# Performance work log

Measured on AMD Instinct MI355X. Metric: run time of the kernel, lower is better.

## Reference

```python
import jax, jax.numpy as jnp
import numpy as np

B = 131072      # batch
IN = 1024       # input_dim
H = 384         # hidden[0]
L = 128         # latent_dim = hidden[1]
K = 32          # slots_k
R = 2           # top_r
TAU = 0.7


def setup_inputs() -> dict:
    key = jax.random.key(0)
    ks = jax.random.split(key, 8)
    s = 0.02
    f32 = jnp.float32
    return {
        "x":  jax.random.normal(ks[0], (B, IN), f32),
        "w1": jax.random.normal(ks[1], (IN, H), f32) * s,
        "b1": jnp.zeros((H,), f32),
        "w2": jax.random.normal(ks[2], (H, L), f32) * s,
        "b2": jnp.zeros((L,), f32),
        "mk": jax.random.normal(ks[3], (K, L), f32) * s,  # memory_keys
        "mv": jax.random.normal(ks[4], (K, L), f32) * s,  # memory_values
        "w3": jax.random.normal(ks[5], (2 * L, H), f32) * s,
        "b3": jnp.zeros((H,), f32),
        "w4": jax.random.normal(ks[6], (H, 1), f32) * s,
        "b4": jnp.zeros((1,), f32),
    }


def reference(x, w1, b1, w2, b2, mk, mv, w3, b3, w4, b4):
    # block_a: Linear -> GELU -> (Dropout=id in eval) -> Linear -> GELU
    z = jax.nn.gelu(x @ w1 + b1, approximate=False)
    z = jax.nn.gelu(z @ w2 + b2, approximate=False)          # [B, L]

    # top-r slot attention over memory bank
    logits = (z @ mk.T) / TAU                                 # [B, K]
    _, idx = jax.lax.top_k(logits, R)                         # [B, R]
    keep = jax.nn.one_hot(idx, K, dtype=logits.dtype).sum(-2) > 0  # [B, K] bool
    masked = jnp.where(keep, logits, -jnp.inf)
    attn = jax.nn.softmax(masked, axis=-1)                    # [B, K]
    mem = attn @ mv                                           # [B, L]

    fused = jnp.concatenate([z, mem], axis=-1)                # [B, 2L]

    # default head: Linear -> GELU -> Linear(.,1)
    h = jax.nn.gelu(fused @ w3 + b3, approximate=False)
    logit = (h @ w4 + b4)[..., 0]                             # [B]
    return jax.nn.sigmoid(logit)
```

## Files before the change

kernel.cpp:

```cpp
#include <hip/hip_runtime.h>

#define BATCH   131072
#define INDIM   1024
#define BM      64
#define BDIM    512
#define NBLK    (BATCH / BM)

#define WT0_OFF  0
#define WT1_OFF  24576
#define XTA_OFF  49152
#define XTB_OFF  57344
#define Z1_OFF   0
#define W2T0_OFF 50176
#define W2T1_OFF 58368
#define FZ_OFF   0
#define RP_OFF   33792
#define W3T_OFF  42240
#define CB_OFF   66816
#define B1S_OFF  (CB_OFF)
#define B2S_OFF  (CB_OFF + 1536)
#define B3S_OFF  (CB_OFF + 2048)
#define W4S_OFF  (CB_OFF + 3584)
#define MKS_OFF  (CB_OFF + 5120)
#define SMEM_BYTES (CB_OFF + 13824)

typedef unsigned short u16;
typedef u16    u16x8  __attribute__((ext_vector_type(8)));
typedef u16    u16x4  __attribute__((ext_vector_type(4)));
typedef __bf16 bf16x8 __attribute__((ext_vector_type(8)));
typedef __bf16 bf16x4 __attribute__((ext_vector_type(4)));
typedef float  f32x4  __attribute__((ext_vector_type(4)));

__device__ __forceinline__ u16 f2bf(float f) {
  unsigned u = __float_as_uint(f);
  u += 0x7FFFu + ((u >> 16) & 1u);
  return (u16)(u >> 16);
}

__device__ __forceinline__ float gelu_fast(float v) {
  float t = v * v;
  float u = v * fmaf(t, 0.0356774081f, 0.7978845608f);
  float e = __builtin_amdgcn_exp2f(u * -2.885390082f);
  return v * __builtin_amdgcn_rcpf(1.0f + e);
}

__device__ __forceinline__ f32x4 mfma16(u16x8 a, u16x8 b, f32x4 c) {
  return __builtin_amdgcn_mfma_f32_16x16x32_bf16(
      __builtin_bit_cast(bf16x8, a), __builtin_bit_cast(bf16x8, b), c, 0, 0, 0);
}

__device__ __forceinline__ u16x8 cvt8(float4 a, float4 b) {
  bf16x8 r;
  r[0]=(__bf16)a.x; r[1]=(__bf16)a.y; r[2]=(__bf16)a.z; r[3]=(__bf16)a.w;
  r[4]=(__bf16)b.x; r[5]=(__bf16)b.y; r[6]=(__bf16)b.z; r[7]=(__bf16)b.w;
  return __builtin_bit_cast(u16x8, r);
}
__device__ __forceinline__ u16x4 cvt4(float4 a) {
  bf16x4 r;
  r[0]=(__bf16)a.x; r[1]=(__bf16)a.y; r[2]=(__bf16)a.z; r[3]=(__bf16)a.w;
  return __builtin_bit_cast(u16x4, r);
}

typedef __attribute__((address_space(3))) unsigned int       lds_u32;
typedef __attribute__((address_space(1))) const unsigned int glb_u32;
__device__ __forceinline__ void gload16(const void* g, void* l) {
  __builtin_amdgcn_global_load_lds((glb_u32*)g, (lds_u32*)l, 16, 0, 0);
}

#define FENCE_SCHED __builtin_amdgcn_sched_barrier(0)
#define WAIT_LGKM0 do { asm volatile("s_waitcnt lgkmcnt(0)" ::: "memory"); FENCE_SCHED; } while (0)
#define WAIT_VMN(N) do { asm volatile("s_waitcnt vmcnt(" #N ")" ::: "memory"); FENCE_SCHED; } while (0)
#define BARRIER_LGKM do { \
  asm volatile("s_waitcnt lgkmcnt(0)" ::: "memory"); \
  __builtin_amdgcn_s_barrier(); FENCE_SCHED; } while (0)

__global__ void prep_kernel(const float* __restrict__ w1, const float* __restrict__ w2,
                            const float* __restrict__ w3, u16* __restrict__ w1s,
                            u16* __restrict__ w2s, u16* __restrict__ w3s) {
  int i = blockIdx.x * 256 + threadIdx.x;
  if (i < 393216) {
    int t = i / 12288, p = i % 12288;
    int r = p >> 5, q = p & 31, cp = q >> 3, o = q & 7;
    int k = t * 32 + ((cp ^ ((r >> 1) & 3)) << 3) + o;
    w1s[i] = f2bf(w1[k * 384 + r]);
  } else if (i < 442368) {
    int j = i - 393216;
    int t = j / 4096, p = j % 4096;
    int r = p >> 5, q = p & 31, cp = q >> 3, o = q & 7;
    int k = t * 32 + ((cp ^ ((r >> 1) & 3)) << 3) + o;
    w2s[j] = f2bf(w2[k * 128 + r]);
  } else if (i < 540672) {
    int j = i - 442368;
    int t = j / 12288, p = j % 12288;
    int r = p >> 5, q = p & 31, cp = q >> 3, o = q & 7;
    int k = t * 32 + ((cp ^ ((r >> 1) & 3)) << 3) + o;
    w3s[j] = f2bf(w3[k * 384 + r]);
  }
}

__global__ __launch_bounds__(BDIM, 4) void fused_kernel(
    const float* __restrict__ x,  const u16* __restrict__ w1s,
    const float* __restrict__ b1, const u16* __restrict__ w2s,
    const float* __restrict__ b2, const float* __restrict__ mkw,
    const float* __restrict__ mvw, const u16* __restrict__ w3s,
    const float* __restrict__ b3, const float* __restrict__ w4,
    const float* __restrict__ b4, float* __restrict__ out) {
  extern __shared__ char smem[];
  u16*   z1  = (u16*)(smem + Z1_OFF);
  u16*   fz  = (u16*)(smem + FZ_OFF);
  u16*   w3t = (u16*)(smem + W3T_OFF);
  u16*   wt0 = (u16*)(smem + WT0_OFF);
  u16*   wt1 = (u16*)(smem + WT1_OFF);
  float* b1s = (float*)(smem + B1S_OFF);
  float* b2s = (float*)(smem + B2S_OFF);
  float* b3s = (float*)(smem + B3S_OFF);
  float* w4s = (float*)(smem + W4S_OFF);
  u16*   mks = (u16*)(smem + MKS_OFF);
  float* rowpart = (float*)(smem + RP_OFF);

  const int tid  = threadIdx.x;
  const int lane = tid & 63;
  const int wid  = tid >> 6;
  const int l15  = lane & 15;
  const int g    = lane >> 4;
  const int sw8  = (g ^ ((l15 >> 1) & 3)) * 8;
  const int row0 = blockIdx.x * BM;
  const int wrow = wid * 48;
  const int wstrip = wid * 1536;

  if (tid < 384) b1s[tid] = b1[tid];
  if (tid < 128) b2s[tid] = b2[tid];
  if (tid < 384) b3s[tid] = b3[tid];
  if (tid < 384) w4s[tid] = w4[tid];
  {
    int r = tid >> 4, cc = (tid & 15) * 8;
    const float4* p = (const float4*)(mkw + r * 128 + cc);
    *(u16x8*)(mks + r * 136 + cc) = cvt8(p[0], p[1]);
  }
  {
    const u16* ws = w1s + wstrip + lane * 8;
    gload16(ws, wt0 + wstrip); gload16(ws + 512, wt0 + wstrip + 512);
    gload16(ws + 1024, wt0 + wstrip + 1024);
    const u16* ws1 = ws + 12288;
    gload16(ws1, wt1 + wstrip); gload16(ws1 + 512, wt1 + wstrip + 512);
    gload16(ws1 + 1024, wt1 + wstrip + 1024);
  }
  FENCE_SCHED;
  const int xrow = tid >> 3, xq = tid & 7;
  const float* xp = x + (long)(row0 + xrow) * INDIM + xq * 4;
  const int xpub = xrow * 32 + (((xq >> 1) ^ ((xrow >> 1) & 3)) << 3) + (xq & 1) * 4;
  float4 xA = *(const float4*)xp, xB = *(const float4*)(xp + 32);
  *(u16x4*)((u16*)(smem + XTA_OFF) + xpub)        = cvt4(xA);
  *(u16x4*)((u16*)(smem + XTA_OFF) + 2048 + xpub) = cvt4(xB);
  xA = *(const float4*)(xp + 64); xB = *(const float4*)(xp + 96);
  BARRIER_LGKM;

  f32x4 acc[4][3];
  #pragma unroll
  for (int m = 0; m < 4; ++m)
    #pragma unroll
    for (int n = 0; n < 3; ++n) acc[m][n] = (f32x4){0.f, 0.f, 0.f, 0.f};

  for (int p = 0; p < 14; ++p) {
    const u16* xrb = (const u16*)(smem + ((p & 1) ? XTB_OFF : XTA_OFF));
    u16* xwb = (u16*)(smem + ((p & 1) ? XTA_OFF : XTB_OFF));
    WAIT_VMN(5);
    {
      u16x8 af[4], bfr[3];
      #pragma unroll
      for (int m = 0; m < 4; ++m) af[m] = *(const u16x8*)(xrb + (m * 16 + l15) * 32 + sw8);
      #pragma unroll
      for (int n = 0; n < 3; ++n) bfr[n] = *(const u16x8*)(wt0 + (wrow + n * 16 + l15) * 32 + sw8);
      WAIT_LGKM0;
      const u16* ws = w1s + (2 * p + 2) * 12288 + wstrip + lane * 8;
      gload16(ws, wt0 + wstrip); gload16(ws + 512, wt0 + wstrip + 512);
      gload16(ws + 1024, wt0 + wstrip + 1024);
      #pragma unroll
      for (int m = 0; m < 4; ++m)
        #pragma unroll
        for (int n = 0; n < 3; ++n) acc[m][n] = mfma16(bfr[n], af[m], acc[m][n]);
    }
    WAIT_VMN(5);
    {
      u16x8 af[4], bfr[3];
      #pragma unroll
      for (int m = 0; m < 4; ++m) af[m] = *(const u16x8*)(xrb + 2048 + (m * 16 + l15) * 32 + sw8);
      #pragma unroll
      for (int n = 0; n < 3; ++n) bfr[n] = *(const u16x8*)(wt1 + (wrow + n * 16 + l15) * 32 + sw8);
      WAIT_LGKM0;
      const u16* ws = w1s + (2 * p + 3) * 12288 + wstrip + lane * 8;
      gload16(ws, wt1 + wstrip); gload16(ws + 512, wt1 + wstrip + 512);
      gload16(ws + 1024, wt1 + wstrip + 1024);
      #pragma unroll
      for (int m = 0; m < 4; ++m)
        #pragma unroll
        for (int n = 0; n < 3; ++n) acc[m][n] = mfma16(bfr[n], af[m], acc[m][n]);
    }
    *(u16x4*)(xwb + xpub)        = cvt4(xA);
    *(u16x4*)(xwb + 2048 + xpub) = cvt4(xB);
    xA = *(const float4*)(xp + (2 * p + 4) * 32);
    xB = *(const float4*)(xp + (2 * p + 5) * 32);
    BARRIER_LGKM;
  }
  {
    const u16* xrb = (const u16*)(smem + XTA_OFF);
    u16* xwb = (u16*)(smem + XTB_OFF);
    WAIT_VMN(5);
    {
      u16x8 af[4], bfr[3];
      #pragma unroll
      for (int m = 0; m < 4; ++m) af[m] = *(const u16x8*)(xrb + (m * 16 + l15) * 32 + sw8);
      #pragma unroll
      for (int n = 0; n < 3; ++n) bfr[n] = *(const u16x8*)(wt0 + (wrow + n * 16 + l15) * 32 + sw8);
      WAIT_LGKM0;
      const u16* ws = w1s + 30 * 12288 + wstrip + lane * 8;
      gload16(ws, wt0 + wstrip); gload16(ws + 512, wt0 + wstrip + 512);
      gload16(ws + 1024, wt0 + wstrip + 1024);
      #pragma unroll
      for (int m = 0; m < 4; ++m)
        #pragma unroll
        for (int n = 0; n < 3; ++n) acc[m][n] = mfma16(bfr[n], af[m], acc[m][n]);
    }
    WAIT_VMN(5);
    {
      u16x8 af[4], bfr[3];
      #pragma unroll
      for (int m = 0; m < 4; ++m) af[m] = *(const u16x8*)(xrb + 2048 + (m * 16 + l15) * 32 + sw8);
      #pragma unroll
      for (int n = 0; n < 3; ++n) bfr[n] = *(const u16x8*)(wt1 + (wrow + n * 16 + l15) * 32 + sw8);
      WAIT_LGKM0;
      const u16* ws = w1s + 31 * 12288 + wstrip + lane * 8;
      gload16(ws, wt1 + wstrip); gload16(ws + 512, wt1 + wstrip + 512);
      gload16(ws + 1024, wt1 + wstrip + 1024);
      #pragma unroll
      for (int m = 0; m < 4; ++m)
        #pragma unroll
        for (int n = 0; n < 3; ++n) acc[m][n] = mfma16(bfr[n], af[m], acc[m][n]);
    }
    *(u16x4*)(xwb + xpub)        = cvt4(xA);
    *(u16x4*)(xwb + 2048 + xpub) = cvt4(xB);
    BARRIER_LGKM;
  }
  {
    const u16* xrb = (const u16*)(smem + XTB_OFF);
    WAIT_VMN(3);
    {
      u16x8 af[4], bfr[3];
      #pragma unroll
      for (int m = 0; m < 4; ++m) af[m] = *(const u16x8*)(xrb + (m * 16 + l15) * 32 + sw8);
      #pragma unroll
      for (int n = 0; n < 3; ++n) bfr[n] = *(const u16x8*)(wt0 + (wrow + n * 16 + l15) * 32 + sw8);
      WAIT_LGKM0;
      #pragma unroll
      for (int m = 0; m < 4; ++m)
        #pragma unroll
        for (int n = 0; n < 3; ++n) acc[m][n] = mfma16(bfr[n], af[m], acc[m][n]);
    }
    WAIT_VMN(0);
    {
      u16x8 af[4], bfr[3];
      #pragma unroll
      for (int m = 0; m < 4; ++m) af[m] = *(const u16x8*)(xrb + 2048 + (m * 16 + l15) * 32 + sw8);
      #pragma unroll
      for (int n = 0; n < 3; ++n) bfr[n] = *(const u16x8*)(wt1 + (wrow + n * 16 + l15) * 32 + sw8);
      WAIT_LGKM0;
      #pragma unroll
      for (int m = 0; m < 4; ++m)
        #pragma unroll
        for (int n = 0; n < 3; ++n) acc[m][n] = mfma16(bfr[n], af[m], acc[m][n]);
    }
  }
  BARRIER_LGKM;

  {
    const u16* s2 = w2s + wid * 512 + lane * 8;
    gload16(s2, (u16*)(smem + W2T0_OFF) + wid * 512);
    const u16* s2b = w2s + 4096 + wid * 512 + lane * 8;
    gload16(s2b, (u16*)(smem + W2T1_OFF) + wid * 512);
  }
  #pragma unroll
  for (int m = 0; m < 4; ++m) {
    #pragma unroll
    for (int n = 0; n < 3; ++n) {
      int col = wrow + n * 16 + g * 4;
      float4 bv = *(const float4*)(b1s + col);
      f32x4 a = acc[m][n];
      float4 gv = {gelu_fast(a[0] + bv.x), gelu_fast(a[1] + bv.y),
                   gelu_fast(a[2] + bv.z), gelu_fast(a[3] + bv.w)};
      *(u16x4*)(z1 + (m * 16 + l15) * 392 + col) = cvt4(gv);
    }
  }
  BARRIER_LGKM;

  f32x4 acc2[4];
  #pragma unroll
  for (int m = 0; m < 4; ++m) acc2[m] = (f32x4){0.f, 0.f, 0.f, 0.f};
  for (int kt = 0; kt < 12; ++kt) {
    if (kt < 10) { WAIT_VMN(1); } else { WAIT_VMN(0); }
    const u16* wb = (const u16*)(smem + ((kt & 1) ? W2T1_OFF : W2T0_OFF));
    u16x8 a2f[4];
    #pragma unroll
    for (int m = 0; m < 4; ++m)
      a2f[m] = *(const u16x8*)(z1 + (m * 16 + l15) * 392 + kt * 32 + g * 8);
    u16x8 b2f = *(const u16x8*)(wb + (wid * 16 + l15) * 32 + sw8);
    WAIT_LGKM0;
    if (kt < 10) {
      const u16* s2 = w2s + (kt + 2) * 4096 + wid * 512 + lane * 8;
      gload16(s2, (u16*)(smem + ((kt & 1) ? W2T1_OFF : W2T0_OFF)) + wid * 512);
    }
    #pragma unroll
    for (int m = 0; m < 4; ++m) acc2[m] = mfma16(b2f, a2f[m], acc2[m]);
  }
  BARRIER_LGKM;

  {
    const u16* s3 = w3s + wid * 1536 + lane * 8;
    u16* d3 = w3t + wid * 1536;
    gload16(s3, d3); gload16(s3 + 512, d3 + 512); gload16(s3 + 1024, d3 + 1024);
  }
  #pragma unroll
  for (int m = 0; m < 4; ++m) {
    int col = wid * 16 + g * 4;
    float4 bv = *(const float4*)(b2s + col);
    f32x4 a = acc2[m];
    float4 gv = {gelu_fast(a[0] + bv.x), gelu_fast(a[1] + bv.y),
                 gelu_fast(a[2] + bv.z), gelu_fast(a[3] + bv.w)};
    *(u16x4*)(fz + (m * 16 + l15) * 264 + col) = cvt4(gv);
  }
  BARRIER_LGKM;

  if (wid < 4) {
    const int wr = wid * 16 + l15;
    f32x4 accl[2] = {(f32x4){0,0,0,0}, (f32x4){0,0,0,0}};
    #pragma unroll
    for (int ks = 0; ks < 4; ++ks) {
      u16x8 afz = *(const u16x8*)(fz + wr * 264 + ks * 32 + g * 8);
      u16x8 k0  = *(const u16x8*)(mks + l15 * 136 + ks * 32 + g * 8);
      u16x8 k1  = *(const u16x8*)(mks + (16 + l15) * 136 + ks * 32 + g * 8);
      accl[0] = mfma16(k0, afz, accl[0]);
      accl[1] = mfma16(k1, afz, accl[1]);
    }
    float m1 = -3.4e38f, m2 = -3.4e38f; int i1 = -1, i2 = -1;
    #pragma unroll
    for (int n = 0; n < 2; ++n)
      #pragma unroll
      for (int j = 0; j < 4; ++j) {
        float v = accl[n][j]; int idx = n * 16 + g * 4 + j;
        if (v > m1) { m2 = m1; i2 = i1; m1 = v; i1 = idx; }
        else if (v > m2) { m2 = v; i2 = idx; }
      }
    #pragma unroll
    for (int d = 16; d <= 32; d <<= 1) {
      float om1 = __shfl_xor(m1, d); int oi1 = __shfl_xor(i1, d);
      float om2 = __shfl_xor(m2, d); int oi2 = __shfl_xor(i2, d);
      bool take = (om1 > m1) || (om1 == m1 && oi1 < i1);
      if (take) {
        float nm2; int ni2;
        if (m1 > om2 || (m1 == om2 && i1 < oi2)) { nm2 = m1; ni2 = i1; }
        else { nm2 = om2; ni2 = oi2; }
        m1 = om1; i1 = oi1; m2 = nm2; i2 = ni2;
      } else {
        if (om1 > m2 || (om1 == m2 && oi1 < i2)) { m2 = om1; i2 = oi1; }
      }
    }
    float a1 = __builtin_amdgcn_rcpf(
        1.0f + __builtin_amdgcn_exp2f((m2 - m1) * (1.44269504f / 0.7f)));
    float a2 = 1.0f - a1;
    const float* v1 = mvw + i1 * 128 + g * 32;
    const float* v2 = mvw + i2 * 128 + g * 32;
    #pragma unroll
    for (int c = 0; c < 4; ++c) {
      float4 A0 = *(const float4*)(v1 + c * 8), A1 = *(const float4*)(v1 + c * 8 + 4);
      float4 B0 = *(const float4*)(v2 + c * 8), B1 = *(const float4*)(v2 + c * 8 + 4);
      float4 r0 = {a1*A0.x + a2*B0.x, a1*A0.y + a2*B0.y, a1*A0.z + a2*B0.z, a1*A0.w + a2*B0.w};
      float4 r1 = {a1*A1.x + a2*B1.x, a1*A1.y + a2*B1.y, a1*A1.z + a2*B1.z, a1*A1.w + a2*B1.w};
      *(u16x8*)(fz + wr * 264 + 128 + g * 32 + c * 8) = cvt8(r0, r1);
    }
  }
  BARRIER_LGKM;

  f32x4 acc3[4][3];
  #pragma unroll
  for (int m = 0; m < 4; ++m)
    #pragma unroll
    for (int n = 0; n < 3; ++n) acc3[m][n] = (f32x4){0.f, 0.f, 0.f, 0.f};
  for (int kt = 0; kt < 8; ++kt) {
    WAIT_VMN(0);
    u16x8 a3f[4], b3f[3];
    #pragma unroll
    for (int m = 0; m < 4; ++m)
      a3f[m] = *(const u16x8*)(fz + (m * 16 + l15) * 264 + kt * 32 + g * 8);
    #pragma unroll
    for (int n = 0; n < 3; ++n)
      b3f[n] = *(const u16x8*)(w3t + (wrow + n * 16 + l15) * 32 + sw8);
    WAIT_LGKM0;
    if (kt < 7) {
      const u16* s3 = w3s + (kt + 1) * 12288 + wid * 1536 + lane * 8;
      u16* d3 = w3t + wid * 1536;
      gload16(s3, d3); gload16(s3 + 512, d3 + 512); gload16(s3 + 1024, d3 + 1024);
    }
    #pragma unroll
    for (int m = 0; m < 4; ++m)
      #pragma unroll
      for (int n = 0; n < 3; ++n) acc3[m][n] = mfma16(b3f[n], a3f[m], acc3[m][n]);
  }

  #pragma unroll
  for (int m = 0; m < 4; ++m) {
    float s = 0.f;
    #pragma unroll
    for (int n = 0; n < 3; ++n) {
      int col = wrow + n * 16 + g * 4;
      float4 bv = *(const float4*)(b3s + col);
      float4 wv = *(const float4*)(w4s + col);
      f32x4 a = acc3[m][n];
      s += gelu_fast(a[0] + bv.x) * wv.x + gelu_fast(a[1] + bv.y) * wv.y +
           gelu_fast(a[2] + bv.z) * wv.z + gelu_fast(a[3] + bv.w) * wv.w;
    }
    s += __shfl_xor(s, 16);
    s += __shfl_xor(s, 32);
    if (lane < 16) rowpart[(m * 16 + l15) * 8 + wid] = s;
  }
  BARRIER_LGKM;
  if (tid < BM) {
    const float4* rp = (const float4*)(rowpart + tid * 8);
    float4 p0 = rp[0], p1 = rp[1];
    float lg = b4[0] + p0.x + p0.y + p0.z + p0.w + p1.x + p1.y + p1.z + p1.w;
    out[row0 + tid] = __builtin_amdgcn_rcpf(1.0f + __builtin_amdgcn_exp2f(-lg * 1.44269504f));
  }
}

extern "C" void kernel_launch(void* const* d_in, const int* in_sizes, int n_in,
                              void* d_out, int out_size, void* d_ws, size_t ws_size,
                              hipStream_t stream) {
  const float* x  = (const float*)d_in[0];
  const float* w1 = (const float*)d_in[1];
  const float* b1 = (const float*)d_in[2];
  const float* w2 = (const float*)d_in[3];
  const float* b2 = (const float*)d_in[4];
  const float* mk = (const float*)d_in[5];
  const float* mv = (const float*)d_in[6];
  const float* w3 = (const float*)d_in[7];
  const float* b3 = (const float*)d_in[8];
  const float* w4 = (const float*)d_in[9];
  const float* b4 = (const float*)d_in[10];

  u16* w1s = (u16*)d_ws;
  u16* w2s = w1s + 393216;
  u16* w3s = w1s + 442368;

  prep_kernel<<<2112, 256, 0, stream>>>(w1, w2, w3, w1s, w2s, w3s);

  (void)hipFuncSetAttribute(reinterpret_cast<const void*>(fused_kernel),
                            hipFuncAttributeMaxDynamicSharedMemorySize, SMEM_BYTES);
  fused_kernel<<<NBLK, BDIM, SMEM_BYTES, stream>>>(x, w1s, b1, w2s, b2, mk, mv, w3s,
                                                   b3, w4, b4, (float*)d_out);
}
```

Measured before the change: 229.0 us.

## Halve block to 4 waves, each wave computing twice the output columns

Result: slower. 237.4 us (+3.7%).

```diff
diff --git a/kernel.cpp b/kernel.cpp
--- a/kernel.cpp
+++ b/kernel.cpp
@@ -3,7 +3,7 @@
 #define BATCH   131072
 #define INDIM   1024
 #define BM      64
-#define BDIM    512
+#define BDIM    256
 #define NBLK    (BATCH / BM)
 
 #define WT0_OFF  0
@@ -98,7 +98,7 @@
   }
 }
 
-__global__ __launch_bounds__(BDIM, 4) void fused_kernel(
+__global__ __launch_bounds__(BDIM, 2) void fused_kernel(
     const float* __restrict__ x,  const u16* __restrict__ w1s,
     const float* __restrict__ b1, const u16* __restrict__ w2s,
     const float* __restrict__ b2, const float* __restrict__ mkw,
@@ -111,6 +111,8 @@
   u16*   w3t = (u16*)(smem + W3T_OFF);
   u16*   wt0 = (u16*)(smem + WT0_OFF);
   u16*   wt1 = (u16*)(smem + WT1_OFF);
+  u16*   w2t0 = (u16*)(smem + W2T0_OFF);
+  u16*   w2t1 = (u16*)(smem + W2T1_OFF);
   float* b1s = (float*)(smem + B1S_OFF);
   float* b2s = (float*)(smem + B2S_OFF);
   float* b3s = (float*)(smem + B3S_OFF);
@@ -125,163 +127,130 @@
   const int g    = lane >> 4;
   const int sw8  = (g ^ ((l15 >> 1) & 3)) * 8;
   const int row0 = blockIdx.x * BM;
-  const int wrow = wid * 48;
-  const int wstrip = wid * 1536;
-
-  if (tid < 384) b1s[tid] = b1[tid];
+  const int wrow = wid * 96;
+  const int wstrip = wid * 3072;
+
+  {
+    const u16* ws = w1s + wstrip + lane * 8;
+    #pragma unroll
+    for (int i = 0; i < 6; ++i) gload16(ws + i * 512, wt0 + wstrip + i * 512);
+    const u16* ws1 = ws + 12288;
+    #pragma unroll
+    for (int i = 0; i < 6; ++i) gload16(ws1 + i * 512, wt1 + wstrip + i * 512);
+  }
+  FENCE_SCHED;
+  const int xrow = tid >> 2, xq = tid & 3;
+  const float* xp = x + (long)(row0 + xrow) * INDIM + xq * 8;
+  const int xpub = xrow * 32 + ((xq ^ ((xrow >> 1) & 3)) << 3);
+  float4 xA0 = *(const float4*)xp,        xA1 = *(const float4*)(xp + 4);
+  float4 xB0 = *(const float4*)(xp + 32), xB1 = *(const float4*)(xp + 36);
+
+  for (int i = tid; i < 384; i += BDIM) b1s[i] = b1[i];
   if (tid < 128) b2s[tid] = b2[tid];
-  if (tid < 384) b3s[tid] = b3[tid];
-  if (tid < 384) w4s[tid] = w4[tid];
-  {
-    int r = tid >> 4, cc = (tid & 15) * 8;
-    const float4* p = (const float4*)(mkw + r * 128 + cc);
-    *(u16x8*)(mks + r * 136 + cc) = cvt8(p[0], p[1]);
-  }
-  {
-    const u16* ws = w1s + wstrip + lane * 8;
-    gload16(ws, wt0 + wstrip); gload16(ws + 512, wt0 + wstrip + 512);
-    gload16(ws + 1024, wt0 + wstrip + 1024);
-    const u16* ws1 = ws + 12288;
-    gload16(ws1, wt1 + wstrip); gload16(ws1 + 512, wt1 + wstrip + 512);
-    gload16(ws1 + 1024, wt1 + wstrip + 1024);
-  }
-  FENCE_SCHED;
-  const int xrow = tid >> 3, xq = tid & 7;
-  const float* xp = x + (long)(row0 + xrow) * INDIM + xq * 4;
-  const int xpub = xrow * 32 + (((xq >> 1) ^ ((xrow >> 1) & 3)) << 3) + (xq & 1) * 4;
-  float4 xA = *(const float4*)xp, xB = *(const float4*)(xp + 32);
-  *(u16x4*)((u16*)(smem + XTA_OFF) + xpub)        = cvt4(xA);
-  *(u16x4*)((u16*)(smem + XTA_OFF) + 2048 + xpub) = cvt4(xB);
-  xA = *(const float4*)(xp + 64); xB = *(const float4*)(xp + 96);
-  BARRIER_LGKM;
-
-  f32x4 acc[4][3];
+  for (int i = tid; i < 384; i += BDIM) b3s[i] = b3[i];
+  for (int i = tid; i < 384; i += BDIM) w4s[i] = w4[i];
+  {
+    int r = tid >> 3, cc = (tid & 7) * 16;
+    const float4* pm = (const float4*)(mkw + r * 128 + cc);
+    *(u16x8*)(mks + r * 136 + cc)     = cvt8(pm[0], pm[1]);
+    *(u16x8*)(mks + r * 136 + cc + 8) = cvt8(pm[2], pm[3]);
+  }
+  *(u16x8*)((u16*)(smem + XTA_OFF) + xpub)        = cvt8(xA0, xA1);
+  *(u16x8*)((u16*)(smem + XTA_OFF) + 2048 + xpub) = cvt8(xB0, xB1);
+  xA0 = *(const float4*)(xp + 64); xA1 = *(const float4*)(xp + 68);
+  xB0 = *(const float4*)(xp + 96); xB1 = *(const float4*)(xp + 100);
+  BARRIER_LGKM;
+
+  f32x4 acc[4][6];
   #pragma unroll
   for (int m = 0; m < 4; ++m)
     #pragma unroll
-    for (int n = 0; n < 3; ++n) acc[m][n] = (f32x4){0.f, 0.f, 0.f, 0.f};
-
-  for (int p = 0; p < 14; ++p) {
+    for (int n = 0; n < 6; ++n) acc[m][n] = (f32x4){0.f, 0.f, 0.f, 0.f};
+
+  for (int p = 0; p < 15; ++p) {
     const u16* xrb = (const u16*)(smem + ((p & 1) ? XTB_OFF : XTA_OFF));
     u16* xwb = (u16*)(smem + ((p & 1) ? XTA_OFF : XTB_OFF));
-    WAIT_VMN(5);
+    WAIT_VMN(10);
     {
-      u16x8 af[4], bfr[3];
+      u16x8 af[4], bfr[6];
       #pragma unroll
       for (int m = 0; m < 4; ++m) af[m] = *(const u16x8*)(xrb + (m * 16 + l15) * 32 + sw8);
       #pragma unroll
-      for (int n = 0; n < 3; ++n) bfr[n] = *(const u16x8*)(wt0 + (wrow + n * 16 + l15) * 32 + sw8);
+      for (int n = 0; n < 6; ++n) bfr[n] = *(const u16x8*)(wt0 + (wrow + n * 16 + l15) * 32 + sw8);
       WAIT_LGKM0;
       const u16* ws = w1s + (2 * p + 2) * 12288 + wstrip + lane * 8;
-      gload16(ws, wt0 + wstrip); gload16(ws + 512, wt0 + wstrip + 512);
-      gload16(ws + 1024, wt0 + wstrip + 1024);
+      #pragma unroll
+      for (int i = 0; i < 6; ++i) gload16(ws + i * 512, wt0 + wstrip + i * 512);
       #pragma unroll
       for (int m = 0; m < 4; ++m)
         #pragma unroll
-        for (int n = 0; n < 3; ++n) acc[m][n] = mfma16(bfr[n], af[m], acc[m][n]);
-    }
-    WAIT_VMN(5);
+        for (int n = 0; n < 6; ++n) acc[m][n] = mfma16(bfr[n], af[m], acc[m][n]);
+    }
+    WAIT_VMN(10);
     {
-      u16x8 af[4], bfr[3];
+      u16x8 af[4], bfr[6];
       #pragma unroll
       for (int m = 0; m < 4; ++m) af[m] = *(const u16x8*)(xrb + 2048 + (m * 16 + l15) * 32 + sw8);
       #pragma unroll
-      for (int n = 0; n < 3; ++n) bfr[n] = *(const u16x8*)(wt1 + (wrow + n * 16 + l15) * 32 + sw8);
+      for (int n = 0; n < 6; ++n) bfr[n] = *(const u16x8*)(wt1 + (wrow + n * 16 + l15) * 32 + sw8);
       WAIT_LGKM0;
       const u16* ws = w1s + (2 * p + 3) * 12288 + wstrip + lane * 8;
-      gload16(ws, wt1 + wstrip); gload16(ws + 512, wt1 + wstrip + 512);
-      gload16(ws + 1024, wt1 + wstrip + 1024);
+      #pragma unroll
+      for (int i = 0; i < 6; ++i) gload16(ws + i * 512, wt1 + wstrip + i * 512);
       #pragma unroll
       for (int m = 0; m < 4; ++m)
         #pragma unroll
-        for (int n = 0; n < 3; ++n) acc[m][n] = mfma16(bfr[n], af[m], acc[m][n]);
-    }
-    *(u16x4*)(xwb + xpub)        = cvt4(xA);
-    *(u16x4*)(xwb + 2048 + xpub) = cvt4(xB);
-    xA = *(const float4*)(xp + (2 * p + 4) * 32);
-    xB = *(const float4*)(xp + (2 * p + 5) * 32);
+        for (int n = 0; n < 6; ++n) acc[m][n] = mfma16(bfr[n], af[m], acc[m][n]);
+    }
+    *(u16x8*)(xwb + xpub)        = cvt8(xA0, xA1);
+    *(u16x8*)(xwb + 2048 + xpub) = cvt8(xB0, xB1);
+    if (p < 14) {
+      xA0 = *(const float4*)(xp + (2 * p + 4) * 32); xA1 = *(const float4*)(xp + (2 * p + 4) * 32 + 4);
+      xB0 = *(const float4*)(xp + (2 * p + 5) * 32); xB1 = *(const float4*)(xp + (2 * p + 5) * 32 + 4);
+    }
     BARRIER_LGKM;
   }
   {
-    const u16* xrb = (const u16*)(smem + XTA_OFF);
-    u16* xwb = (u16*)(smem + XTB_OFF);
-    WAIT_VMN(5);
+    const u16* xrb = (const u16*)(smem + XTB_OFF);
+    WAIT_VMN(6);
     {
-      u16x8 af[4], bfr[3];
+      u16x8 af[4], bfr[6];
       #pragma unroll
       for (int m = 0; m < 4; ++m) af[m] = *(const u16x8*)(xrb + (m * 16 + l15) * 32 + sw8);
       #pragma unroll
-      for (int n = 0; n < 3; ++n) bfr[n] = *(const u16x8*)(wt0 + (wrow + n * 16 + l15) * 32 + sw8);
+      for (int n = 0; n < 6; ++n) bfr[n] = *(const u16x8*)(wt0 + (wrow + n * 16 + l15) * 32 + sw8);
       WAIT_LGKM0;
-      const u16* ws = w1s + 30 * 12288 + wstrip + lane * 8;
-      gload16(ws, wt0 + wstrip); gload16(ws + 512, wt0 + wstrip + 512);
-      gload16(ws + 1024, wt0 + wstrip + 1024);
       #pragma unroll
       for (int m = 0; m < 4; ++m)
         #pragma unroll
-        for (int n = 0; n < 3; ++n) acc[m][n] = mfma16(bfr[n], af[m], acc[m][n]);
-    }
-    WAIT_VMN(5);
+        for (int n = 0; n < 6; ++n) acc[m][n] = mfma16(bfr[n], af[m], acc[m][n]);
+    }
+    WAIT_VMN(0);
     {
-      u16x8 af[4], bfr[3];
+      u16x8 af[4], bfr[6];
       #pragma unroll
       for (int m = 0; m < 4; ++m) af[m] = *(const u16x8*)(xrb + 2048 + (m * 16 + l15) * 32 + sw8);
       #pragma unroll
-      for (int n = 0; n < 3; ++n) bfr[n] = *(const u16x8*)(wt1 + (wrow + n * 16 + l15) * 32 + sw8);
+      for (int n = 0; n < 6; ++n) bfr[n] = *(const u16x8*)(wt1 + (wrow + n * 16 + l15) * 32 + sw8);
       WAIT_LGKM0;
-      const u16* ws = w1s + 31 * 12288 + wstrip + lane * 8;
-      gload16(ws, wt1 + wstrip); gload16(ws + 512, wt1 + wstrip + 512);
-      gload16(ws + 1024, wt1 + wstrip + 1024);
       #pragma unroll
       for (int m = 0; m < 4; ++m)
         #pragma unroll
-        for (int n = 0; n < 3; ++n) acc[m][n] = mfma16(bfr[n], af[m], acc[m][n]);
-    }
-    *(u16x4*)(xwb + xpub)        = cvt4(xA);
-    *(u16x4*)(xwb + 2048 + xpub) = cvt4(xB);
-    BARRIER_LGKM;
-  }
-  {
-    const u16* xrb = (const u16*)(smem + XTB_OFF);
-    WAIT_VMN(3);
-    {
-      u16x8 af[4], bfr[3];
-      #pragma unroll
-      for (int m = 0; m < 4; ++m) af[m] = *(const u16x8*)(xrb + (m * 16 + l15) * 32 + sw8);
-      #pragma unroll
-      for (int n = 0; n < 3; ++n) bfr[n] = *(const u16x8*)(wt0 + (wrow + n * 16 + l15) * 32 + sw8);
-      WAIT_LGKM0;
-      #pragma unroll
-      for (int m = 0; m < 4; ++m)
-        #pragma unroll
-        for (int n = 0; n < 3; ++n) acc[m][n] = mfma16(bfr[n], af[m], acc[m][n]);
-    }
-    WAIT_VMN(0);
-    {
-      u16x8 af[4], bfr[3];
-      #pragma unroll
-      for (int m = 0; m < 4; ++m) af[m] = *(const u16x8*)(xrb + 2048 + (m * 16 + l15) * 32 + sw8);
-      #pragma unroll
-      for (int n = 0; n < 3; ++n) bfr[n] = *(const u16x8*)(wt1 + (wrow + n * 16 + l15) * 32 + sw8);
-      WAIT_LGKM0;
-      #pragma unroll
-      for (int m = 0; m < 4; ++m)
-        #pragma unroll
-        for (int n = 0; n < 3; ++n) acc[m][n] = mfma16(bfr[n], af[m], acc[m][n]);
-    }
-  }
-  BARRIER_LGKM;
-
-  {
-    const u16* s2 = w2s + wid * 512 + lane * 8;
-    gload16(s2, (u16*)(smem + W2T0_OFF) + wid * 512);
-    const u16* s2b = w2s + 4096 + wid * 512 + lane * 8;
-    gload16(s2b, (u16*)(smem + W2T1_OFF) + wid * 512);
+        for (int n = 0; n < 6; ++n) acc[m][n] = mfma16(bfr[n], af[m], acc[m][n]);
+    }
+  }
+  BARRIER_LGKM;
+
+  {
+    const u16* s2 = w2s + wid * 1024 + lane * 8;
+    gload16(s2, w2t0 + wid * 1024); gload16(s2 + 512, w2t0 + wid * 1024 + 512);
+    const u16* s2b = w2s + 4096 + wid * 1024 + lane * 8;
+    gload16(s2b, w2t1 + wid * 1024); gload16(s2b + 512, w2t1 + wid * 1024 + 512);
   }
   #pragma unroll
   for (int m = 0; m < 4; ++m) {
     #pragma unroll
-    for (int n = 0; n < 3; ++n) {
+    for (int n = 0; n < 6; ++n) {
       int col = wrow + n * 16 + g * 4;
       float4 bv = *(const float4*)(b1s + col);
       f32x4 a = acc[m][n];
@@ -292,44 +261,52 @@
   }
   BARRIER_LGKM;
 
-  f32x4 acc2[4];
-  #pragma unroll
-  for (int m = 0; m < 4; ++m) acc2[m] = (f32x4){0.f, 0.f, 0.f, 0.f};
+  f32x4 acc2[4][2];
+  #pragma unroll
+  for (int m = 0; m < 4; ++m) { acc2[m][0] = (f32x4){0,0,0,0}; acc2[m][1] = (f32x4){0,0,0,0}; }
   for (int kt = 0; kt < 12; ++kt) {
-    if (kt < 10) { WAIT_VMN(1); } else { WAIT_VMN(0); }
-    const u16* wb = (const u16*)(smem + ((kt & 1) ? W2T1_OFF : W2T0_OFF));
-    u16x8 a2f[4];
+    if (kt < 11) { WAIT_VMN(2); } else { WAIT_VMN(0); }
+    const u16* wb = (kt & 1) ? w2t1 : w2t0;
+    u16x8 a2f[4], b2f[2];
     #pragma unroll
     for (int m = 0; m < 4; ++m)
       a2f[m] = *(const u16x8*)(z1 + (m * 16 + l15) * 392 + kt * 32 + g * 8);
-    u16x8 b2f = *(const u16x8*)(wb + (wid * 16 + l15) * 32 + sw8);
+    #pragma unroll
+    for (int n = 0; n < 2; ++n)
+      b2f[n] = *(const u16x8*)(wb + (wid * 32 + n * 16 + l15) * 32 + sw8);
     WAIT_LGKM0;
     if (kt < 10) {
-      const u16* s2 = w2s + (kt + 2) * 4096 + wid * 512 + lane * 8;
-      gload16(s2, (u16*)(smem + ((kt & 1) ? W2T1_OFF : W2T0_OFF)) + wid * 512);
-    }
-    #pragma unroll
-    for (int m = 0; m < 4; ++m) acc2[m] = mfma16(b2f, a2f[m], acc2[m]);
-  }
-  BARRIER_LGKM;
-
-  {
-    const u16* s3 = w3s + wid * 1536 + lane * 8;
-    u16* d3 = w3t + wid * 1536;
-    gload16(s3, d3); gload16(s3 + 512, d3 + 512); gload16(s3 + 1024, d3 + 1024);
+      const u16* s2 = w2s + (kt + 2) * 4096 + wid * 1024 + lane * 8;
+      u16* d2 = ((kt & 1) ? w2t1 : w2t0) + wid * 1024;
+      gload16(s2, d2); gload16(s2 + 512, d2 + 512);
+    }
+    #pragma unroll
+    for (int m = 0; m < 4; ++m)
+      #pragma unroll
+      for (int n = 0; n < 2; ++n) acc2[m][n] = mfma16(b2f[n], a2f[m], acc2[m][n]);
+  }
+  BARRIER_LGKM;
+
+  {
+    const u16* s3 = w3s + wstrip + lane * 8;
+    #pragma unroll
+    for (int i = 0; i < 6; ++i) gload16(s3 + i * 512, w3t + wstrip + i * 512);
   }
   #pragma unroll
   for (int m = 0; m < 4; ++m) {
-    int col = wid * 16 + g * 4;
-    float4 bv = *(const float4*)(b2s + col);
-    f32x4 a = acc2[m];
-    float4 gv = {gelu_fast(a[0] + bv.x), gelu_fast(a[1] + bv.y),
-                 gelu_fast(a[2] + bv.z), gelu_fast(a[3] + bv.w)};
-    *(u16x4*)(fz + (m * 16 + l15) * 264 + col) = cvt4(gv);
-  }
-  BARRIER_LGKM;
-
-  if (wid < 4) {
+    #pragma unroll
+    for (int n = 0; n < 2; ++n) {
+      int col = wid * 32 + n * 16 + g * 4;
+      float4 bv = *(const float4*)(b2s + col);
+      f32x4 a = acc2[m][n];
+      float4 gv = {gelu_fast(a[0] + bv.x), gelu_fast(a[1] + bv.y),
+                   gelu_fast(a[2] + bv.z), gelu_fast(a[3] + bv.w)};
+      *(u16x4*)(fz + (m * 16 + l15) * 264 + col) = cvt4(gv);
+    }
+  }
+  BARRIER_LGKM;
+
+  {
     const int wr = wid * 16 + l15;
     f32x4 accl[2] = {(f32x4){0,0,0,0}, (f32x4){0,0,0,0}};
     #pragma unroll
@@ -379,37 +356,37 @@
   }
   BARRIER_LGKM;
 
-  f32x4 acc3[4][3];
+  f32x4 acc3[4][6];
   #pragma unroll
   for (int m = 0; m < 4; ++m)
     #pragma unroll
-    for (int n = 0; n < 3; ++n) acc3[m][n] = (f32x4){0.f, 0.f, 0.f, 0.f};
+    for (int n = 0; n < 6; ++n) acc3[m][n] = (f32x4){0.f, 0.f, 0.f, 0.f};
   for (int kt = 0; kt < 8; ++kt) {
     WAIT_VMN(0);
-    u16x8 a3f[4], b3f[3];
+    u16x8 a3f[4], b3f[6];
     #pragma unroll
     for (int m = 0; m < 4; ++m)
       a3f[m] = *(const u16x8*)(fz + (m * 16 + l15) * 264 + kt * 32 + g * 8);
     #pragma unroll
-    for (int n = 0; n < 3; ++n)
+    for (int n = 0; n < 6; ++n)
       b3f[n] = *(const u16x8*)(w3t + (wrow + n * 16 + l15) * 32 + sw8);
     WAIT_LGKM0;
     if (kt < 7) {
-      const u16* s3 = w3s + (kt + 1) * 12288 + wid * 1536 + lane * 8;
-      u16* d3 = w3t + wid * 1536;
-      gload16(s3, d3); gload16(s3 + 512, d3 + 512); gload16(s3 + 1024, d3 + 1024);
+      const u16* s3 = w3s + (kt + 1) * 12288 + wstrip + lane * 8;
+      #pragma unroll
+      for (int i = 0; i < 6; ++i) gload16(s3 + i * 512, w3t + wstrip + i * 512);
     }
     #pragma unroll
     for (int m = 0; m < 4; ++m)
       #pragma unroll
-      for (int n = 0; n < 3; ++n) acc3[m][n] = mfma16(b3f[n], a3f[m], acc3[m][n]);
+      for (int n = 0; n < 6; ++n) acc3[m][n] = mfma16(b3f[n], a3f[m], acc3[m][n]);
   }
 
   #pragma unroll
   for (int m = 0; m < 4; ++m) {
     float s = 0.f;
     #pragma unroll
-    for (int n = 0; n < 3; ++n) {
+    for (int n = 0; n < 6; ++n) {
       int col = wrow + n * 16 + g * 4;
       float4 bv = *(const float4*)(b3s + col);
       float4 wv = *(const float4*)(w4s + col);
@@ -419,13 +396,13 @@
     }
     s += __shfl_xor(s, 16);
     s += __shfl_xor(s, 32);
-    if (lane < 16) rowpart[(m * 16 + l15) * 8 + wid] = s;
+    if (lane < 16) rowpart[(m * 16 + l15) * 4 + wid] = s;
   }
   BARRIER_LGKM;
   if (tid < BM) {
-    const float4* rp = (const float4*)(rowpart + tid * 8);
-    float4 p0 = rp[0], p1 = rp[1];
-    float lg = b4[0] + p0.x + p0.y + p0.z + p0.w + p1.x + p1.y + p1.z + p1.w;
+    const float4* rp = (const float4*)(rowpart + tid * 4);
+    float4 p0 = rp[0];
+    float lg = b4[0] + p0.x + p0.y + p0.z + p0.w;
     out[row0 + tid] = __builtin_amdgcn_rcpf(1.0f + __builtin_amdgcn_exp2f(-lg * 1.44269504f));
   }
 }
```
